# Kernel optimization log

Measured on AMD Instinct MI355X. Metric: run time of the kernel, lower is better.

The kernel has to match this reference:

```python
import jax, jax.numpy as jnp
import numpy as np

B, T, D_IN, D_PROJ = 256, 2048, 25, 128


def setup_inputs() -> dict:
    key = jax.random.key(0)
    ks = jax.random.split(key, 7)
    s1 = 1.0 / np.sqrt(D_IN)
    s2 = 1.0 / np.sqrt(D_PROJ)
    return {
        "x": jax.random.normal(ks[0], (B, T, D_IN), dtype=jnp.float32),
        "ln_gamma": jnp.ones((D_IN,), dtype=jnp.float32),
        "ln_beta": jnp.zeros((D_IN,), dtype=jnp.float32),
        "w1": jax.random.uniform(ks[1], (D_IN, D_PROJ), jnp.float32, -s1, s1),
        "b1": jax.random.uniform(ks[2], (D_PROJ,), jnp.float32, -s1, s1),
        "w2": jax.random.uniform(ks[3], (D_PROJ, D_PROJ), jnp.float32, -s2, s2),
        "b2": jax.random.uniform(ks[4], (D_PROJ,), jnp.float32, -s2, s2),
    }


def reference(x, ln_gamma, ln_beta, w1, b1, w2, b2):
    # LayerNorm over last dim (eps=1e-5, torch default)
    mu = jnp.mean(x, axis=-1, keepdims=True)
    var = jnp.mean(jnp.square(x - mu), axis=-1, keepdims=True)
    xn = (x - mu) * jax.lax.rsqrt(var + 1e-5) * ln_gamma + ln_beta
    h = jnp.einsum("btd,dp->btp", xn, w1) + b1
    h = jax.nn.gelu(h, approximate=False)  # torch nn.GELU default = exact erf
    return jnp.einsum("btp,pq->btq", h, w2) + b2
```

## Files before the change

kernel.cpp:

```cpp
#include <hip/hip_runtime.h>
#include <hip/hip_bf16.h>
#include <stdint.h>

#define BT    (256*2048)
#define DIN   25
#define DP    128
#define MTILE 128
#define NBLK  (BT/MTILE)
#define HSTR  136
#define WREG  (32*HSTR*2)
#define XOFF  4608
#define SM_BYTES (4*WREG)

typedef __attribute__((ext_vector_type(8))) __bf16          bf16x8;
typedef __attribute__((ext_vector_type(8))) unsigned short  u16x8;
typedef __attribute__((ext_vector_type(4))) float           f32x4;

__device__ __forceinline__ unsigned short f2bf(float f) {
  unsigned int u = __float_as_uint(f);
  u += 0x7fffu + ((u >> 16) & 1u);
  return (unsigned short)(u >> 16);
}

__device__ __forceinline__ float gelu_exact(float x) {
  float z  = 0.70710678118654752f * x;
  float az = __builtin_fabsf(z);
  float t  = __builtin_amdgcn_rcpf(1.0f + 0.3275911f * az);
  float p  = t*(0.254829592f + t*(-0.284496736f + t*(1.421413741f +
             t*(-1.453152027f + t*1.061405429f))));
  float e  = __expf(-z*z);
  float erf_az = 1.0f - p*e;
  float erf_z  = (x < 0.f) ? -erf_az : erf_az;
  return 0.5f * x * (1.0f + erf_z);
}

__device__ __forceinline__ void async16(void* lds, const void* g) {
  __builtin_amdgcn_global_load_lds(
      (const __attribute__((address_space(1))) unsigned int*)g,
      (__attribute__((address_space(3)))       unsigned int*)lds, 16, 0, 0);
}

__global__ void prep_kernel(const float* __restrict__ w1, const float* __restrict__ w2,
                            unsigned short* __restrict__ wf) {
  int idx = blockIdx.x * 256 + threadIdx.x;
  if (idx >= 40 * 512) return;
  int f = idx >> 9, r = idx & 511, l = r >> 3, j = r & 7;
  float val;
  if (f < 8) {
    int k = (l >> 4) * 8 + j;
    int n = f * 16 + (l & 15);
    val = (k < DIN) ? w1[k * DP + n] : 0.f;
  } else {
    int g = f - 8, nt = g >> 2, ks = g & 3;
    int k = ks * 32 + (l >> 4) * 8 + j;
    int n = nt * 16 + (l & 15);
    val = w2[k * DP + n];
  }
  wf[idx] = f2bf(val);
}

__global__ __launch_bounds__(256, 4) void fused_kernel(
    const float* __restrict__ x,   const float* __restrict__ gam,
    const float* __restrict__ bet, const float* __restrict__ b1,
    const float* __restrict__ b2,  const unsigned short* __restrict__ wfr,
    float* __restrict__ out) {
  __shared__ __align__(16) unsigned char smem[SM_BYTES];
  const int tid  = threadIdx.x;
  const int lane = tid & 63, w = tid >> 6;
  const int quad = lane >> 4, l15 = lane & 15;
  const int kbase = quad * 8;
  const long long rowW = (long long)blockIdx.x * MTILE + w * 32;
  unsigned char* wbase = smem + w * WREG;
  const unsigned char* wfb = (const unsigned char*)wfr;

  {
    const long long xoff0 = rowW * (DIN * 4);
    const long long xmax  = (long long)BT * DIN * 4 - 16;
#pragma unroll
    for (int i = 0; i < 4; i++) {
      long long off = xoff0 + (long long)(i * 64 + lane) * 16;
      if (off > xmax) off = xmax;
      async16(wbase + XOFF + i * 1024 + lane * 16, (const unsigned char*)x + off);
    }
  }

  float gk[8], bk[8];
#pragma unroll
  for (int j = 0; j < 8; j++) {
    int k = kbase + j;
    bool v = (k < DIN);
    gk[j] = v ? gam[k] : 0.f;
    bk[j] = v ? bet[k] : 0.f;
  }
  bf16x8 wb1[8];
#pragma unroll
  for (int nt = 0; nt < 8; nt++)
    wb1[nt] = *(const bf16x8*)(wfb + nt * 1024 + lane * 16);

  asm volatile("s_waitcnt vmcnt(0)" ::: "memory");
  __builtin_amdgcn_sched_barrier(0);

  const float* xs = (const float*)(wbase + XOFF);
  bf16x8 afrag[2];
#pragma unroll
  for (int t = 0; t < 2; t++) {
    float xv[8];
    float s = 0.f;
#pragma unroll
    for (int j = 0; j < 8; j++) {
      int k = kbase + j;
      float v = 0.f;
      if (k < DIN) v = xs[(t * 16 + l15) * DIN + k];
      xv[j] = v;
      s += v;
    }
    s += __shfl_xor(s, 16);  s += __shfl_xor(s, 32);
    float mu = s * (1.f / DIN);
    float vv = 0.f;
#pragma unroll
    for (int j = 0; j < 8; j++) {
      int k = kbase + j;
      float d = (k < DIN) ? (xv[j] - mu) : 0.f;
      vv += d * d;
    }
    vv += __shfl_xor(vv, 16); vv += __shfl_xor(vv, 32);
    float inv = rsqrtf(vv * (1.f / DIN) + 1e-5f);
    u16x8 pk;
#pragma unroll
    for (int j = 0; j < 8; j++)
      pk[j] = f2bf((xv[j] - mu) * inv * gk[j] + bk[j]);
    afrag[t] = __builtin_bit_cast(bf16x8, pk);
  }

  float b1v[8];
#pragma unroll
  for (int nt = 0; nt < 8; nt++) b1v[nt] = b1[nt * 16 + l15];

  unsigned short* hb = (unsigned short*)wbase;
  const f32x4 zf = {0.f, 0.f, 0.f, 0.f};
#pragma unroll
  for (int t = 0; t < 2; t++) {
    f32x4 acc[8];
#pragma unroll
    for (int nt = 0; nt < 8; nt++)
      acc[nt] = __builtin_amdgcn_mfma_f32_16x16x32_bf16(afrag[t], wb1[nt], zf, 0, 0, 0);
#pragma unroll
    for (int nt = 0; nt < 8; nt++) {
      float bias = b1v[nt];
      int col = nt * 16 + l15;
#pragma unroll
      for (int r = 0; r < 4; r++) {
        int row = t * 16 + quad * 4 + r;
        hb[row * HSTR + col] = f2bf(gelu_exact(acc[nt][r] + bias));
      }
    }
  }

  asm volatile("s_waitcnt lgkmcnt(0)" ::: "memory");
  __builtin_amdgcn_sched_barrier(0);

  bf16x8 af[2][4];
#pragma unroll
  for (int t = 0; t < 2; t++)
#pragma unroll
    for (int ks = 0; ks < 4; ks++)
      af[t][ks] = *(const bf16x8*)((const unsigned char*)hb +
                    (t * 16 + l15) * (HSTR * 2) + ks * 64 + quad * 16);

  float b2v[8];
#pragma unroll
  for (int nt = 0; nt < 8; nt++) b2v[nt] = b2[nt * 16 + l15];

  float* orow = out + rowW * DP;
#pragma unroll
  for (int nt = 0; nt < 8; nt++) {
    bf16x8 wq[4];
#pragma unroll
    for (int ks = 0; ks < 4; ks++)
      wq[ks] = *(const bf16x8*)(wfb + 8192 + (nt * 4 + ks) * 1024 + lane * 16);
    f32x4 a0 = zf, a1 = zf;
#pragma unroll
    for (int ks = 0; ks < 4; ks++) {
      a0 = __builtin_amdgcn_mfma_f32_16x16x32_bf16(af[0][ks], wq[ks], a0, 0, 0, 0);
      a1 = __builtin_amdgcn_mfma_f32_16x16x32_bf16(af[1][ks], wq[ks], a1, 0, 0, 0);
    }
    int col = nt * 16 + l15;
    float bias = b2v[nt];
#pragma unroll
    for (int r = 0; r < 4; r++) {
      int rr = quad * 4 + r;
      orow[(long long)(rr)      * DP + col] = a0[r] + bias;
      orow[(long long)(rr + 16) * DP + col] = a1[r] + bias;
    }
  }
}

extern "C" void kernel_launch(void* const* d_in, const int* in_sizes, int n_in,
                              void* d_out, int out_size, void* d_ws, size_t ws_size,
                              hipStream_t stream) {
  const float* x   = (const float*)d_in[0];
  const float* gam = (const float*)d_in[1];
  const float* bet = (const float*)d_in[2];
  const float* w1  = (const float*)d_in[3];
  const float* b1  = (const float*)d_in[4];
  const float* w2  = (const float*)d_in[5];
  const float* b2  = (const float*)d_in[6];
  float* out = (float*)d_out;
  unsigned short* wf = (unsigned short*)d_ws;

  prep_kernel<<<80, 256, 0, stream>>>(w1, w2, wf);
  fused_kernel<<<NBLK, 256, 0, stream>>>(x, gam, bet, b1, b2, wf, out);
}
```

Baseline: 363.9 us.

## Split second GEMM by output columns across waves with block-shared hidden tile

```diff
diff --git a/kernel.cpp b/kernel.cpp
--- a/kernel.cpp
+++ b/kernel.cpp
@@ -13,7 +13,6 @@
 #define SM_BYTES (4*WREG)
 
 typedef __attribute__((ext_vector_type(8))) __bf16          bf16x8;
-typedef __attribute__((ext_vector_type(8))) unsigned short  u16x8;
 typedef __attribute__((ext_vector_type(4))) float           f32x4;
 
 __device__ __forceinline__ unsigned short f2bf(float f) {
@@ -70,7 +69,7 @@
   const int quad = lane >> 4, l15 = lane & 15;
   const int kbase = quad * 8;
   const long long rowW = (long long)blockIdx.x * MTILE + w * 32;
-  unsigned char* wbase = smem + w * WREG;
+  unsigned char* wband = smem + w * WREG;
   const unsigned char* wfb = (const unsigned char*)wfr;
 
   {
@@ -80,7 +79,7 @@
     for (int i = 0; i < 4; i++) {
       long long off = xoff0 + (long long)(i * 64 + lane) * 16;
       if (off > xmax) off = xmax;
-      async16(wbase + XOFF + i * 1024 + lane * 16, (const unsigned char*)x + off);
+      async16(wband + XOFF + i * 1024 + lane * 16, (const unsigned char*)x + off);
     }
   }
 
@@ -96,11 +95,14 @@
 #pragma unroll
   for (int nt = 0; nt < 8; nt++)
     wb1[nt] = *(const bf16x8*)(wfb + nt * 1024 + lane * 16);
+  float b1v[8];
+#pragma unroll
+  for (int nt = 0; nt < 8; nt++) b1v[nt] = b1[nt * 16 + l15];
 
   asm volatile("s_waitcnt vmcnt(0)" ::: "memory");
   __builtin_amdgcn_sched_barrier(0);
 
-  const float* xs = (const float*)(wbase + XOFF);
+  const float* xs = (const float*)(wband + XOFF);
   bf16x8 afrag[2];
 #pragma unroll
   for (int t = 0; t < 2; t++) {
@@ -125,72 +127,83 @@
     }
     vv += __shfl_xor(vv, 16); vv += __shfl_xor(vv, 32);
     float inv = rsqrtf(vv * (1.f / DIN) + 1e-5f);
-    u16x8 pk;
+    bf16x8 av;
 #pragma unroll
     for (int j = 0; j < 8; j++)
-      pk[j] = f2bf((xv[j] - mu) * inv * gk[j] + bk[j]);
-    afrag[t] = __builtin_bit_cast(bf16x8, pk);
-  }
-
-  float b1v[8];
-#pragma unroll
-  for (int nt = 0; nt < 8; nt++) b1v[nt] = b1[nt * 16 + l15];
-
-  unsigned short* hb = (unsigned short*)wbase;
+      av[j] = (__bf16)((xv[j] - mu) * inv * gk[j] + bk[j]);
+    afrag[t] = av;
+  }
+
+  __bf16* hbb = (__bf16*)smem;
+  const int hrow0 = w * 32;
   const f32x4 zf = {0.f, 0.f, 0.f, 0.f};
-#pragma unroll
-  for (int t = 0; t < 2; t++) {
+  {
     f32x4 acc[8];
 #pragma unroll
     for (int nt = 0; nt < 8; nt++)
-      acc[nt] = __builtin_amdgcn_mfma_f32_16x16x32_bf16(afrag[t], wb1[nt], zf, 0, 0, 0);
+      acc[nt] = __builtin_amdgcn_mfma_f32_16x16x32_bf16(afrag[0], wb1[nt], zf, 0, 0, 0);
 #pragma unroll
     for (int nt = 0; nt < 8; nt++) {
       float bias = b1v[nt];
       int col = nt * 16 + l15;
 #pragma unroll
       for (int r = 0; r < 4; r++) {
-        int row = t * 16 + quad * 4 + r;
-        hb[row * HSTR + col] = f2bf(gelu_exact(acc[nt][r] + bias));
+        int row = hrow0 + quad * 4 + r;
+        hbb[row * HSTR + col] = (__bf16)gelu_exact(acc[nt][r] + bias);
       }
     }
   }
 
-  asm volatile("s_waitcnt lgkmcnt(0)" ::: "memory");
-  __builtin_amdgcn_sched_barrier(0);
-
-  bf16x8 af[2][4];
-#pragma unroll
-  for (int t = 0; t < 2; t++)
+  bf16x8 wb2[2][4];
+  float bias2[2];
+  {
+    f32x4 acc[8];
+#pragma unroll
+    for (int nt = 0; nt < 8; nt++)
+      acc[nt] = __builtin_amdgcn_mfma_f32_16x16x32_bf16(afrag[1], wb1[nt], zf, 0, 0, 0);
+#pragma unroll
+    for (int ni = 0; ni < 2; ni++) {
+#pragma unroll
+      for (int ks = 0; ks < 4; ks++)
+        wb2[ni][ks] = *(const bf16x8*)(wfb + 8192 + (((w * 2 + ni) * 4) + ks) * 1024 + lane * 16);
+      bias2[ni] = b2[(w * 2 + ni) * 16 + l15];
+    }
+#pragma unroll
+    for (int nt = 0; nt < 8; nt++) {
+      float bias = b1v[nt];
+      int col = nt * 16 + l15;
+#pragma unroll
+      for (int r = 0; r < 4; r++) {
+        int row = hrow0 + 16 + quad * 4 + r;
+        hbb[row * HSTR + col] = (__bf16)gelu_exact(acc[nt][r] + bias);
+      }
+    }
+  }
+
+  __syncthreads();
+
+  const long long orow0 = (long long)blockIdx.x * MTILE;
+  const int c0 = (w * 2 + 0) * 16 + l15;
+  const int c1 = (w * 2 + 1) * 16 + l15;
+#pragma unroll
+  for (int mt = 0; mt < 8; mt++) {
+    bf16x8 af[4];
 #pragma unroll
     for (int ks = 0; ks < 4; ks++)
-      af[t][ks] = *(const bf16x8*)((const unsigned char*)hb +
-                    (t * 16 + l15) * (HSTR * 2) + ks * 64 + quad * 16);
-
-  float b2v[8];
-#pragma unroll
-  for (int nt = 0; nt < 8; nt++) b2v[nt] = b2[nt * 16 + l15];
-
-  float* orow = out + rowW * DP;
-#pragma unroll
-  for (int nt = 0; nt < 8; nt++) {
-    bf16x8 wq[4];
-#pragma unroll
-    for (int ks = 0; ks < 4; ks++)
-      wq[ks] = *(const bf16x8*)(wfb + 8192 + (nt * 4 + ks) * 1024 + lane * 16);
+      af[ks] = *(const bf16x8*)((const unsigned char*)smem +
+                 (mt * 16 + l15) * (HSTR * 2) + ks * 64 + quad * 16);
     f32x4 a0 = zf, a1 = zf;
 #pragma unroll
     for (int ks = 0; ks < 4; ks++) {
-      a0 = __builtin_amdgcn_mfma_f32_16x16x32_bf16(af[0][ks], wq[ks], a0, 0, 0, 0);
-      a1 = __builtin_amdgcn_mfma_f32_16x16x32_bf16(af[1][ks], wq[ks], a1, 0, 0, 0);
-    }
-    int col = nt * 16 + l15;
-    float bias = b2v[nt];
+      a0 = __builtin_amdgcn_mfma_f32_16x16x32_bf16(af[ks], wb2[0][ks], a0, 0, 0, 0);
+      a1 = __builtin_amdgcn_mfma_f32_16x16x32_bf16(af[ks], wb2[1][ks], a1, 0, 0, 0);
+    }
+    float* orow = out + (orow0 + mt * 16) * DP;
 #pragma unroll
     for (int r = 0; r < 4; r++) {
-      int rr = quad * 4 + r;
-      orow[(long long)(rr)      * DP + col] = a0[r] + bias;
-      orow[(long long)(rr + 16) * DP + col] = a1[r] + bias;
+      int row = quad * 4 + r;
+      orow[row * DP + c0] = a0[r] + bias2[0];
+      orow[row * DP + c1] = a1[r] + bias2[1];
     }
   }
 }
```

New measurement: 345.1 us. -5.2%, faster.
